# Kernel optimization log

Hardware: AMD Instinct MI355X
Metric: run time of the kernel (lower is better)

Reference implementation:

```python
import jax, jax.numpy as jnp
import numpy as np

N = 16384      # nodes per graph (128x128 image)
E = 9 * N      # 8-neighborhood + self edges
C = 512        # input feature channels
M = 32         # matrixSize


def _p(key, shape, scale=0.05):
    return jax.random.normal(key, shape, dtype=jnp.float32) * scale


def setup_inputs() -> dict:
    key = jax.random.key(0)
    ks = jax.random.split(key, 40)
    inp = {
        "cF": jax.random.normal(ks[0], (N, C), dtype=jnp.float32),
        "sF": jax.random.normal(ks[1], (N, C), dtype=jnp.float32),
        "content_edge_index": jax.random.randint(ks[2], (2, E), 0, N),
        "content_selections": jax.random.randint(ks[3], (E,), 0, 9),
        "style_edge_index": jax.random.randint(ks[4], (2, E), 0, N),
        "style_selections": jax.random.randint(ks[5], (E,), 0, 9),
        "compress_W": _p(ks[6], (1, C, M)),   # kernel_size=1 -> 1 selection
        "compress_b": _p(ks[7], (M,)),
        "unzip_W": _p(ks[8], (1, M, C)),
        "unzip_b": _p(ks[9], (C,)),
    }
    i = 10
    for net in ("cnet", "snet"):
        for j, (ci, co) in enumerate([(C, 256), (256, 128), (128, M)], 1):
            inp[f"{net}_W{j}"] = _p(ks[i], (9, ci, co)); i += 1  # kernel_size=3 -> 9 selections
            inp[f"{net}_b{j}"] = _p(ks[i], (co,)); i += 1
        inp[f"{net}_fcW"] = _p(ks[i], (M * M, M * M)); i += 1   # torch Linear [out,in]
        inp[f"{net}_fcb"] = _p(ks[i], (M * M,)); i += 1
    return inp


def sel_conv(x, edge_index, sel, W, b):
    """SelectionConv: per-selection weight, gather from src, scatter-add to dst.
    x: [N,Cin], W: [S,Cin,Cout]. Edges with selection >= S are masked (kernel_size=1)."""
    S = W.shape[0]
    t = jnp.einsum('nc,scd->snd', x, W)              # [S, N, Cout]
    src, dst = edge_index[0], edge_index[1]
    msgs = t[jnp.minimum(sel, S - 1), src]           # [E, Cout]
    msgs = jnp.where((sel < S)[:, None], msgs, 0.0)
    return jax.ops.segment_sum(msgs, dst, num_segments=x.shape[0]) + b


def cnn_net(x, ei, sel, W1, b1, W2, b2, W3, b3, fcW, fcb):
    h = jax.nn.relu(sel_conv(x, ei, sel, W1, b1))
    h = jax.nn.relu(sel_conv(h, ei, sel, W2, b2))
    h = sel_conv(h, ei, sel, W3, b3)                 # [N, M]
    g = (h.T @ h) / h.shape[0]                       # [M, M] gram
    return g.reshape(-1) @ fcW.T + fcb               # [M*M]


def reference(cF, sF, content_edge_index, content_selections, style_edge_index,
              style_selections, compress_W, compress_b, unzip_W, unzip_b,
              cnet_W1, cnet_b1, cnet_W2, cnet_b2, cnet_W3, cnet_b3, cnet_fcW, cnet_fcb,
              snet_W1, snet_b1, snet_W2, snet_b2, snet_W3, snet_b3, snet_fcW, snet_fcb):
    cMean = jnp.mean(cF, axis=0, keepdims=True)
    cFc = cF - cMean
    sMean = jnp.mean(sF, axis=0, keepdims=True)
    sFc = sF - sMean
    compress_content = sel_conv(cFc, content_edge_index, content_selections,
                                compress_W, compress_b)          # [N, M]
    m = compress_W.shape[2]
    cMat = cnn_net(cFc, content_edge_index, content_selections,
                   cnet_W1, cnet_b1, cnet_W2, cnet_b2, cnet_W3, cnet_b3,
                   cnet_fcW, cnet_fcb).reshape(m, m)
    sMat = cnn_net(sFc, style_edge_index, style_selections,
                   snet_W1, snet_b1, snet_W2, snet_b2, snet_W3, snet_b3,
                   snet_fcW, snet_fcb).reshape(m, m)
    transmatrix = sMat @ cMat                                    # [M, M]
    transfeature = (transmatrix @ compress_content.T).T          # [N, M]
    out = sel_conv(transfeature, content_edge_index, content_selections,
                   unzip_W, unzip_b) + sMean                     # [N, 512]
    return (out, transmatrix)
```

## Files before the change

### kernel.cpp

```cpp
#include <hip/hip_runtime.h>
#include <hip/hip_bf16.h>
#include <cstddef>
#include <cstdint>

#define NN 16384
#define EE (9*NN)
#define CC 512

typedef __attribute__((ext_vector_type(4))) float f32x4;
typedef __attribute__((ext_vector_type(8))) short bf16x8;

static inline int idiv(int a, int b){ return (a+b-1)/b; }

__device__ __forceinline__ float bf2f(unsigned short u){
    union{unsigned u; float f;} v; v.u = ((unsigned)u) << 16; return v.f;
}
__device__ __forceinline__ unsigned short f2bf(float f){
    union{float f; unsigned u;} v; v.f = f;
    unsigned r = v.u + 0x7fffu + ((v.u >> 16) & 1u);
    return (unsigned short)(r >> 16);
}

__device__ __forceinline__ void gload16(const void* gsrc, void* ldst){
    __builtin_amdgcn_global_load_lds(
        (const __attribute__((address_space(1))) unsigned int*)gsrc,
        (__attribute__((address_space(3))) unsigned int*)ldst,
        16, 0, 0);
}


__global__ void zero_i(int* __restrict__ p, int n){
    int i = blockIdx.x*256 + threadIdx.x; if (i < n) p[i] = 0;
}

__global__ void colsum2(const float* __restrict__ F0, float* __restrict__ cs0,
                        const float* __restrict__ F1, float* __restrict__ cs1){
    const float* F = blockIdx.z ? F1 : F0;
    float* cs = blockIdx.z ? cs1 : cs0;
    const int RPB = NN/256;
    int r0 = blockIdx.x * RPB;
    int c4 = threadIdx.x;
    float4 s = {0.f,0.f,0.f,0.f};
    for (int r = 0; r < RPB; ++r){
        float4 v = ((const float4*)(F + (size_t)(r0+r)*CC))[c4];
        s.x += v.x; s.y += v.y; s.z += v.z; s.w += v.w;
    }
    atomicAdd(&cs[c4*4+0], s.x);
    atomicAdd(&cs[c4*4+1], s.y);
    atomicAdd(&cs[c4*4+2], s.z);
    atomicAdd(&cs[c4*4+3], s.w);
}

__global__ void center2(const float* __restrict__ F0, const float* __restrict__ cs0,
                        ushort4* __restrict__ o0,
                        const float* __restrict__ F1, const float* __restrict__ cs1,
                        ushort4* __restrict__ o1){
    const float* F = blockIdx.z ? F1 : F0;
    const float* cs = blockIdx.z ? cs1 : cs0;
    ushort4* o = blockIdx.z ? o1 : o0;
    int i = blockIdx.x*256 + threadIdx.x;
    float4 v = ((const float4*)F)[i];
    int c = (i << 2) & (CC-1);
    float4 m = *(const float4*)(cs + c);
    ushort4 r;
    r.x = f2bf(v.x - m.x*(1.f/NN));
    r.y = f2bf(v.y - m.y*(1.f/NN));
    r.z = f2bf(v.z - m.z*(1.f/NN));
    r.w = f2bf(v.w - m.w*(1.f/NN));
    o[i] = r;
}

__global__ void wtransz(const float* __restrict__ W0, unsigned short* __restrict__ Wt0,
                        const float* __restrict__ W1, unsigned short* __restrict__ Wt1,
                        int S, int K, int Cout, int Npad, int Kpad){
    const float* W = blockIdx.z ? W1 : W0;
    unsigned short* Wt = blockIdx.z ? Wt1 : Wt0;
    int idx = blockIdx.x*256 + threadIdx.x;
    if (idx >= Npad*Kpad) return;
    int colp = idx / Kpad, k = idx - colp*Kpad;
    int s = colp / Cout, j = colp - s*Cout;
    float v = 0.f;
    if (s < S && k < K) v = W[((size_t)s*K + k)*Cout + j];
    Wt[idx] = f2bf(v);
}

__global__ void wtrans2z(const float* __restrict__ W0, const float* __restrict__ W1,
                         unsigned short* __restrict__ Wt0, unsigned short* __restrict__ Wt1,
                         int K, int Cout){
    __shared__ float tile[32][129];
    int s = blockIdx.z % 9;
    const float* W = (blockIdx.z < 9) ? W0 : W1;
    unsigned short* Wt = (blockIdx.z < 9) ? Wt0 : Wt1;
    int jb = blockIdx.x*128, kb = blockIdx.y*32;
    const float* Ws = W + (size_t)s*K*Cout;
    for (int r = 0; r < 32; ++r)
        tile[r][threadIdx.x] = Ws[(size_t)(kb+r)*Cout + jb + threadIdx.x];
    __syncthreads();
    int kk = threadIdx.x & 31, j0 = threadIdx.x >> 5;
    for (int jj = j0; jj < 128; jj += 4)
        Wt[(size_t)(s*Cout + jb + jj)*K + kb + kk] = f2bf(tile[kk][jj]);
}

__global__ void csr_count3(const int* __restrict__ cDst, const int* __restrict__ sDst,
                           const int* __restrict__ cSel,
                           int* __restrict__ cCnt, int* __restrict__ sCnt, int* __restrict__ cCnt0){
    int e = blockIdx.x*256 + threadIdx.x;
    if (e >= EE) return;
    int z = blockIdx.z;
    if (z == 0)      atomicAdd(&cCnt[cDst[e]], 1);
    else if (z == 1) atomicAdd(&sCnt[sDst[e]], 1);
    else if (cSel[e] == 0) atomicAdd(&cCnt0[cDst[e]], 1);
}
__global__ void csr_scan3(const int* __restrict__ c0, const int* __restrict__ c1,
                          const int* __restrict__ c2,
                          int* __restrict__ r0, int* __restrict__ r1, int* __restrict__ r2){
    const int* cnt = blockIdx.z==0 ? c0 : (blockIdx.z==1 ? c1 : c2);
    int* rowptr    = blockIdx.z==0 ? r0 : (blockIdx.z==1 ? r1 : r2);
    __shared__ int part[1024];
    int t = threadIdx.x;
    int base = t*16, s = 0;
    int local[16];
    #pragma unroll
    for (int i = 0; i < 16; ++i){ local[i] = s; s += cnt[base+i]; }
    part[t] = s; __syncthreads();
    for (int off = 1; off < 1024; off <<= 1){
        int v = (t >= off) ? part[t-off] : 0;
        __syncthreads();
        part[t] += v;
        __syncthreads();
    }
    int pre = (t == 0) ? 0 : part[t-1];
    #pragma unroll
    for (int i = 0; i < 16; ++i) rowptr[base+i] = pre + local[i];
    if (t == 1023) rowptr[NN] = part[1023];
}
__global__ void csr_fill3(const int* __restrict__ cSrc, const int* __restrict__ cDst,
                          const int* __restrict__ cSel,
                          const int* __restrict__ sSrc, const int* __restrict__ sDst,
                          const int* __restrict__ sSel,
                          const int* __restrict__ cRow, const int* __restrict__ sRow,
                          const int* __restrict__ cRow0,
                          int* __restrict__ cCur, int* __restrict__ sCur, int* __restrict__ cCur0,
                          int* __restrict__ cEl, int* __restrict__ sEl, int* __restrict__ cEl0){
    int e = blockIdx.x*256 + threadIdx.x;
    if (e >= EE) return;
    int z = blockIdx.z;
    if (z == 0){
        int d = cDst[e];
        int p = atomicAdd(&cCur[d], 1);
        cEl[cRow[d] + p] = (cSrc[e] << 4) | cSel[e];
    } else if (z == 1){
        int d = sDst[e];
        int p = atomicAdd(&sCur[d], 1);
        sEl[sRow[d] + p] = (sSrc[e] << 4) | sSel[e];
    } else if (cSel[e] == 0){
        int d = cDst[e];
        int p = atomicAdd(&cCur0[d], 1);
        cEl0[cRow0[d] + p] = cSrc[e];
    }
}

template<typename OutT>
__global__ __launch_bounds__(256, 2)
void mfma_gemm(const unsigned short* __restrict__ A0, const unsigned short* __restrict__ Bt0,
               OutT* __restrict__ C0,
               const unsigned short* __restrict__ A1, const unsigned short* __restrict__ Bt1,
               OutT* __restrict__ C1, int K, int N){
    const unsigned short* A  = blockIdx.z ? A1 : A0;
    const unsigned short* Bt = blockIdx.z ? Bt1 : Bt0;
    OutT* C = blockIdx.z ? C1 : C0;
    __shared__ __align__(16) unsigned short As[128*64];
    __shared__ __align__(16) unsigned short Bs[128*64];
    const int tid  = threadIdx.x;
    const int wave = tid >> 6, lane = tid & 63;
    const int row0 = blockIdx.y << 7, col0 = blockIdx.x << 7;
    const int wm = wave >> 1, wn = wave & 1;
    const int fr = lane & 15, fq = lane >> 4;
    f32x4 acc[4][4] = {};
    for (int k0 = 0; k0 < K; k0 += 64){
        __syncthreads();
        #pragma unroll
        for (int i = 0; i < 4; ++i){
            int chb = (wave*4 + i) * 64;
            int ch  = chb + lane;
            int r   = ch >> 3, c8 = ch & 7;
            gload16((const char*)(A  + (size_t)(row0 + r)*K + k0) + c8*16, As + chb*8);
            gload16((const char*)(Bt + (size_t)(col0 + r)*K + k0) + c8*16, Bs + chb*8);
        }
        __syncthreads();
        #pragma unroll
        for (int ks = 0; ks < 2; ++ks){
            bf16x8 av[4], bv[4];
            #pragma unroll
            for (int m = 0; m < 4; ++m)
                av[m] = *(const bf16x8*)(As + ((wm<<6)+(m<<4)+fr)*64 + (ks<<5) + (fq<<3));
            #pragma unroll
            for (int n = 0; n < 4; ++n)
                bv[n] = *(const bf16x8*)(Bs + ((wn<<6)+(n<<4)+fr)*64 + (ks<<5) + (fq<<3));
            #pragma unroll
            for (int m = 0; m < 4; ++m)
                #pragma unroll
                for (int n = 0; n < 4; ++n)
                    acc[m][n] = __builtin_amdgcn_mfma_f32_16x16x32_bf16(bv[n], av[m], acc[m][n], 0, 0, 0);
        }
    }
    #pragma unroll
    for (int m = 0; m < 4; ++m){
        int row = row0 + (wm<<6) + (m<<4) + fr;
        OutT* crow = C + (size_t)row*N + col0 + (wn<<6) + (fq<<2);
        #pragma unroll
        for (int n = 0; n < 4; ++n){
            if constexpr (sizeof(OutT) == 2){
                unsigned lo = f2bf(acc[m][n][0]) | ((unsigned)f2bf(acc[m][n][1]) << 16);
                unsigned hi = f2bf(acc[m][n][2]) | ((unsigned)f2bf(acc[m][n][3]) << 16);
                uint2 pk; pk.x = lo; pk.y = hi;
                *(uint2*)((unsigned short*)crow + (n<<4)) = pk;
            } else {
                float4 pk; pk.x = acc[m][n][0]; pk.y = acc[m][n][1];
                pk.z = acc[m][n][2]; pk.w = acc[m][n][3];
                *(float4*)((float*)crow + (n<<4)) = pk;
            }
        }
    }
}

template<int NT, typename OutT>
__global__ __launch_bounds__(256, 4)
void gemm_db(const unsigned short* __restrict__ A0, const unsigned short* __restrict__ Bt0,
             OutT* __restrict__ C0,
             const unsigned short* __restrict__ A1, const unsigned short* __restrict__ Bt1,
             OutT* __restrict__ C1, int N){
    constexpr int LDK = NT*32;
    const unsigned short* A  = blockIdx.z ? A1 : A0;
    const unsigned short* Bt = blockIdx.z ? Bt1 : Bt0;
    OutT* C = blockIdx.z ? C1 : C0;
    __shared__ __align__(16) unsigned short lds[2][2][4096];
    const int tid = threadIdx.x, w = tid >> 6, l = tid & 63;
    const int wm = w >> 1, wn = w & 1;
    const int fr = l & 15, fq = l >> 4;
    const int nbx = gridDim.x;
    const int nwg = gridDim.x * gridDim.y;
    int blin = blockIdx.y * nbx + blockIdx.x;
    int sw = (blin & 7) * (nwg >> 3) + (blin >> 3);
    const int bx = sw % nbx, by = sw / nbx;
    const int row0 = by << 7, col0 = bx << 7;

    const unsigned short* gA = A + (size_t)row0 * LDK;
    const unsigned short* gB = Bt + (size_t)col0 * LDK;

    auto STG = [&](int buf, int t){
        #pragma unroll
        for (int mtx = 0; mtx < 2; ++mtx){
            const unsigned short* gb = mtx ? gB : gA;
            #pragma unroll
            for (int ld = 0; ld < 2; ++ld){
                int o = (ld*256 + tid) * 16;
                int row = o >> 6;
                int kb = (o & 63) ^ (((o >> 7) & 3) << 4);
                gload16((const char*)(gb + (size_t)row*LDK + t*32) + kb,
                        (char*)&lds[buf][mtx][0] + o);
            }
        }
    };

    f32x4 acc[4][4] = {};
    STG(0, 0);
    __syncthreads();
    for (int t = 0; t < NT; ++t){
        int cur = t & 1;
        if (t + 1 < NT) STG(cur ^ 1, t + 1);
        bf16x8 av[4], bv[4];
        #pragma unroll
        for (int m = 0; m < 4; ++m){
            int r = wm*64 + m*16 + fr;
            int p = (r*64 + fq*16) ^ (((r >> 1) & 3) << 4);
            av[m] = *(const bf16x8*)((const char*)&lds[cur][0][0] + p);
        }
        #pragma unroll
        for (int n = 0; n < 4; ++n){
            int r = wn*64 + n*16 + fr;
            int p = (r*64 + fq*16) ^ (((r >> 1) & 3) << 4);
            bv[n] = *(const bf16x8*)((const char*)&lds[cur][1][0] + p);
        }
        #pragma unroll
        for (int m = 0; m < 4; ++m)
            #pragma unroll
            for (int n = 0; n < 4; ++n)
                acc[m][n] = __builtin_amdgcn_mfma_f32_16x16x32_bf16(bv[n], av[m], acc[m][n], 0, 0, 0);
        __syncthreads();
    }

    #pragma unroll
    for (int m = 0; m < 4; ++m){
        int row = row0 + wm*64 + m*16 + fr;
        OutT* crow = C + (size_t)row*N + col0 + (wn<<6) + (fq<<2);
        #pragma unroll
        for (int n = 0; n < 4; ++n){
            if constexpr (sizeof(OutT) == 2){
                unsigned lo = f2bf(acc[m][n][0]) | ((unsigned)f2bf(acc[m][n][1]) << 16);
                unsigned hi = f2bf(acc[m][n][2]) | ((unsigned)f2bf(acc[m][n][3]) << 16);
                uint2 pk; pk.x = lo; pk.y = hi;
                *(uint2*)((unsigned short*)crow + (n<<4)) = pk;
            } else {
                float4 pk; pk.x = acc[m][n][0]; pk.y = acc[m][n][1];
                pk.z = acc[m][n][2]; pk.w = acc[m][n][3];
                *(float4*)((float*)crow + (n<<4)) = pk;
            }
        }
    }
}

template<typename TO, bool RELU>
__global__ void gather8z(const int* __restrict__ rp0, const int* __restrict__ el0,
                         const unsigned short* __restrict__ t0, const float* __restrict__ b0,
                         TO* __restrict__ o0,
                         const int* __restrict__ rp1, const int* __restrict__ el1,
                         const unsigned short* __restrict__ t1, const float* __restrict__ b1,
                         TO* __restrict__ o1,
                         int tStride, int coutShift){
    const int* rowptr = blockIdx.z ? rp1 : rp0;
    const int* elist  = blockIdx.z ? el1 : el0;
    const unsigned short* t = blockIdx.z ? t1 : t0;
    const float* bias = blockIdx.z ? b1 : b0;
    TO* out = blockIdx.z ? o1 : o0;
    int idx = blockIdx.x*256 + threadIdx.x;
    int chSh = coutShift - 3;
    int d = idx >> chSh;
    int c0 = (idx & ((1 << chSh) - 1)) << 3;
    float acc[8];
    {
        const float4* bb = (const float4*)(bias + c0);
        float4 a = bb[0], b = bb[1];
        acc[0]=a.x; acc[1]=a.y; acc[2]=a.z; acc[3]=a.w;
        acc[4]=b.x; acc[5]=b.y; acc[6]=b.z; acc[7]=b.w;
    }
    int j1 = rowptr[d+1];
    #pragma unroll 2
    for (int j = rowptr[d]; j < j1; ++j){
        int p = elist[j];
        int s = p & 15, sr = p >> 4;
        bf16x8 v = *(const bf16x8*)(t + (size_t)sr*tStride + (s << coutShift) + c0);
        #pragma unroll
        for (int k = 0; k < 8; ++k) acc[k] += bf2f((unsigned short)v[k]);
    }
    if (RELU){
        #pragma unroll
        for (int k = 0; k < 8; ++k) acc[k] = fmaxf(acc[k], 0.f);
    }
    if constexpr (sizeof(TO) == 2){
        union { bf16x8 v; unsigned short u[8]; } r;
        #pragma unroll
        for (int k = 0; k < 8; ++k) r.u[k] = f2bf(acc[k]);
        *(bf16x8*)((unsigned short*)out + ((size_t)d << coutShift) + c0) = r.v;
    } else {
        float4 a = {acc[0],acc[1],acc[2],acc[3]};
        float4 b = {acc[4],acc[5],acc[6],acc[7]};
        float4* op = (float4*)((float*)out + ((size_t)d << coutShift) + c0);
        op[0] = a; op[1] = b;
    }
}

template<bool ADDV>
__global__ void gather4f(const int* __restrict__ rowptr, const int* __restrict__ elist,
                         const float* __restrict__ t,
                         const float* __restrict__ bias, const float* __restrict__ addvec,
                         float* __restrict__ out, int tStride, int coutShift){
    int idx = blockIdx.x*256 + threadIdx.x;
    int chSh = coutShift - 2;
    int d = idx >> chSh;
    int c0 = (idx & ((1 << chSh) - 1)) << 2;
    float4 bb = *(const float4*)(bias + c0);
    float acc0 = bb.x, acc1 = bb.y, acc2 = bb.z, acc3 = bb.w;
    if (ADDV){
        float4 av = *(const float4*)(addvec + c0);
        acc0 += av.x*(1.f/NN); acc1 += av.y*(1.f/NN);
        acc2 += av.z*(1.f/NN); acc3 += av.w*(1.f/NN);
    }
    int j1 = rowptr[d+1];
    #pragma unroll 2
    for (int j = rowptr[d]; j < j1; ++j){
        int sr = elist[j];
        float4 v = *(const float4*)(t + (size_t)sr*tStride + c0);
        acc0 += v.x; acc1 += v.y; acc2 += v.z; acc3 += v.w;
    }
    float4 r = {acc0, acc1, acc2, acc3};
    *(float4*)(out + ((size_t)d << coutShift) + c0) = r;
}

__global__ void gram2(const float* __restrict__ h0, float* __restrict__ g0,
                      const float* __restrict__ h1, float* __restrict__ g1){
    const float* h = blockIdx.z ? h1 : h0;
    float* g = blockIdx.z ? g1 : g0;
    const int RPB = NN/64;
    int r0 = blockIdx.x*RPB;
    int i = threadIdx.x >> 5, j = threadIdx.x & 31;
    float s = 0.f;
    for (int r = 0; r < RPB; ++r){
        const float* row = h + (size_t)(r0+r)*32;
        s += row[i]*row[j];
    }
    atomicAdd(&g[threadIdx.x], s);
}

__global__ void fc2(const float* __restrict__ g0, const float* __restrict__ fcW0,
                    const float* __restrict__ fcb0, float* __restrict__ o0,
                    const float* __restrict__ g1, const float* __restrict__ fcW1,
                    const float* __restrict__ fcb1, float* __restrict__ o1){
    const float* g   = blockIdx.z ? g1 : g0;
    const float* fcW = blockIdx.z ? fcW1 : fcW0;
    const float* fcb = blockIdx.z ? fcb1 : fcb0;
    float* outMat    = blockIdx.z ? o1 : o0;
    int i = blockIdx.x;
    float s = 0.f;
    for (int j = threadIdx.x; j < 1024; j += 256)
        s += g[j] * (1.f/NN) * fcW[(size_t)i*1024 + j];
    __shared__ float red[256];
    red[threadIdx.x] = s; __syncthreads();
    for (int off = 128; off > 0; off >>= 1){
        if (threadIdx.x < off) red[threadIdx.x] += red[threadIdx.x+off];
        __syncthreads();
    }
    if (threadIdx.x == 0) outMat[i] = red[0] + fcb[i];
}

__global__ void mm32_kernel(const float* __restrict__ A, const float* __restrict__ B,
                            float* __restrict__ T){
    int i = threadIdx.x >> 5, j = threadIdx.x & 31;
    float s = 0.f;
    for (int k = 0; k < 32; ++k) s += A[i*32+k]*B[k*32+j];
    T[threadIdx.x] = s;
}

__global__ void tf_cvt_kernel(const float* __restrict__ cc, const float* __restrict__ T,
                              unsigned short* __restrict__ tfbB){
    __shared__ float Ts[1024];
    for (int i = threadIdx.x; i < 1024; i += blockDim.x) Ts[i] = T[i];
    __syncthreads();
    int idx = blockIdx.x*blockDim.x + threadIdx.x;
    int n = idx >> 5, i = idx & 31;
    float s = 0.f;
    const float* crow = cc + (size_t)n*32;
    #pragma unroll
    for (int j = 0; j < 32; ++j) s += crow[j] * Ts[i*32+j];
    tfbB[(size_t)n*64 + i] = f2bf(s);
    tfbB[(size_t)n*64 + 32 + i] = 0;
}

extern "C" void kernel_launch(void* const* d_in, const int* in_sizes, int n_in,
                              void* d_out, int out_size, void* d_ws, size_t ws_size,
                              hipStream_t stream){
    const float* cF   = (const float*)d_in[0];
    const float* sF   = (const float*)d_in[1];
    const int*   cEI  = (const int*)d_in[2];
    const int*   cSel = (const int*)d_in[3];
    const int*   sEI  = (const int*)d_in[4];
    const int*   sSel = (const int*)d_in[5];
    const float* compW= (const float*)d_in[6];
    const float* compB= (const float*)d_in[7];
    const float* unzW = (const float*)d_in[8];
    const float* unzB = (const float*)d_in[9];
    const float* cW1=(const float*)d_in[10]; const float* cB1=(const float*)d_in[11];
    const float* cW2=(const float*)d_in[12]; const float* cB2=(const float*)d_in[13];
    const float* cW3=(const float*)d_in[14]; const float* cB3=(const float*)d_in[15];
    const float* cFW=(const float*)d_in[16]; const float* cFB=(const float*)d_in[17];
    const float* sW1=(const float*)d_in[18]; const float* sB1=(const float*)d_in[19];
    const float* sW2=(const float*)d_in[20]; const float* sB2=(const float*)d_in[21];
    const float* sW3=(const float*)d_in[22]; const float* sB3=(const float*)d_in[23];
    const float* sFW=(const float*)d_in[24]; const float* sFB=(const float*)d_in[25];

    float* out  = (float*)d_out;
    float* Tmat = out + (size_t)NN*CC;

    char* w = (char*)d_ws;
    auto alloc = [&](size_t b)->char*{ char* p = w; w += (b + 255) & ~(size_t)255; return p; };
    float* cCol = (float*)alloc(512*4);
    float* sCol = (float*)alloc(512*4);
    float* cg   = (float*)alloc(1024*4);
    float* sg   = (float*)alloc(1024*4);
    float* cMat = (float*)alloc(1024*4);
    float* sMat = (float*)alloc(1024*4);
    int* cCnt = (int*)alloc(NN*4);
    int* cCur = (int*)alloc(NN*4);
    int* sCnt = (int*)alloc(NN*4);
    int* sCur = (int*)alloc(NN*4);
    int* cCnt0= (int*)alloc(NN*4);
    int* cCur0= (int*)alloc(NN*4);
    int* cRow = (int*)alloc((NN+1)*4);
    int* sRow = (int*)alloc((NN+1)*4);
    int* cRow0= (int*)alloc((NN+1)*4);
    int* cEl  = (int*)alloc(EE*4);
    int* sEl  = (int*)alloc(EE*4);
    int* cEl0 = (int*)alloc(EE*4);
    float* ccbuf = (float*)alloc((size_t)NN*32*4);
    unsigned short* tfbB = (unsigned short*)alloc((size_t)NN*64*2);
    unsigned short* wtC1 = (unsigned short*)alloc((size_t)2304*512*2);
    unsigned short* wtC2 = (unsigned short*)alloc((size_t)1280*256*2);
    unsigned short* wtC3 = (unsigned short*)alloc((size_t)384*128*2);
    unsigned short* wtS1 = (unsigned short*)alloc((size_t)2304*512*2);
    unsigned short* wtS2 = (unsigned short*)alloc((size_t)1280*256*2);
    unsigned short* wtS3 = (unsigned short*)alloc((size_t)384*128*2);
    unsigned short* wtCo = (unsigned short*)alloc((size_t)128*512*2);
    unsigned short* wtU  = (unsigned short*)alloc((size_t)512*64*2);
    unsigned short* cFcB = (unsigned short*)alloc((size_t)NN*512*2);
    unsigned short* sFcB = (unsigned short*)alloc((size_t)NN*512*2);
    float* h3c = (float*)alloc((size_t)NN*32*4);
    float* h3s = (float*)alloc((size_t)NN*32*4);
    unsigned short* tC = (unsigned short*)alloc((size_t)NN*2304*2);
    unsigned short* tS = (unsigned short*)alloc((size_t)NN*2304*2);
    float* tFc = (float*)tC;
    unsigned short* h1c = cFcB;
    unsigned short* h1s = sFcB;
    unsigned short* h2c = cFcB + (size_t)NN*256;
    unsigned short* h2s = sFcB + (size_t)NN*256;

    const int* cSrc = cEI; const int* cDst = cEI + EE;
    const int* sSrc = sEI; const int* sDst = sEI + EE;

    int zeroInts = (int)(((char*)cCur0 - (char*)d_ws)/4) + NN;
    zero_i<<<idiv(zeroInts,256),256,0,stream>>>((int*)d_ws, zeroInts);

    colsum2<<<dim3(256,1,2),128,0,stream>>>(cF, cCol, sF, sCol);
    center2<<<dim3(NN*CC/1024,1,2),256,0,stream>>>(cF, cCol, (ushort4*)cFcB,
                                                   sF, sCol, (ushort4*)sFcB);

    wtrans2z<<<dim3(2,16,18),128,0,stream>>>(cW1, sW1, wtC1, wtS1, 512, 256);
    wtrans2z<<<dim3(1,8,18),128,0,stream>>>(cW2, sW2, wtC2, wtS2, 256, 128);
    wtransz<<<dim3(idiv(384*128,256),1,2),256,0,stream>>>(cW3, wtC3, sW3, wtS3, 9,128,32, 384,128);
    wtransz<<<dim3(idiv(128*512,256),1,1),256,0,stream>>>(compW, wtCo, compW, wtCo, 1,512,32, 128,512);
    wtransz<<<dim3(idiv(512*64,256),1,1),256,0,stream>>>(unzW, wtU, unzW, wtU, 1,32,512, 512,64);

    csr_count3<<<dim3(idiv(EE,256),1,3),256,0,stream>>>(cDst, sDst, cSel, cCnt, sCnt, cCnt0);
    csr_scan3<<<dim3(1,1,3),1024,0,stream>>>(cCnt, sCnt, cCnt0, cRow, sRow, cRow0);
    csr_fill3<<<dim3(idiv(EE,256),1,3),256,0,stream>>>(cSrc,cDst,cSel, sSrc,sDst,sSel,
                                                       cRow,sRow,cRow0, cCur,sCur,cCur0,
                                                       cEl,sEl,cEl0);

    mfma_gemm<float><<<dim3(1,128,1),256,0,stream>>>(cFcB, wtCo, tFc,
                                                     cFcB, wtCo, tFc, 512, 128);
    gather4f<false><<<NN*8/256,256,0,stream>>>(cRow0,cEl0,tFc,compB,nullptr,ccbuf,128,5);

    gemm_db<16,unsigned short><<<dim3(18,128,2),256,0,stream>>>(cFcB, wtC1, tC,
                                                                sFcB, wtS1, tS, 2304);
    gather8z<unsigned short,true><<<dim3(2048,1,2),256,0,stream>>>(
        cRow,cEl,tC,cB1,h1c, sRow,sEl,tS,sB1,h1s, 2304, 8);
    gemm_db<8,unsigned short><<<dim3(10,128,2),256,0,stream>>>(h1c, wtC2, tC,
                                                               h1s, wtS2, tS, 1280);
    gather8z<unsigned short,true><<<dim3(1024,1,2),256,0,stream>>>(
        cRow,cEl,tC,cB2,h2c, sRow,sEl,tS,sB2,h2s, 1280, 7);
    mfma_gemm<unsigned short><<<dim3(3,128,2),256,0,stream>>>(h2c, wtC3, tC,
                                                              h2s, wtS3, tS, 128, 384);
    gather8z<float,false><<<dim3(256,1,2),256,0,stream>>>(
        cRow,cEl,tC,cB3,h3c, sRow,sEl,tS,sB3,h3s, 384, 5);
    gram2<<<dim3(64,1,2),1024,0,stream>>>(h3c, cg, h3s, sg);
    fc2<<<dim3(1024,1,2),256,0,stream>>>(cg,cFW,cFB,cMat, sg,sFW,sFB,sMat);

    mm32_kernel<<<1,1024,0,stream>>>(sMat, cMat, Tmat);
    tf_cvt_kernel<<<NN*32/256,256,0,stream>>>(ccbuf, Tmat, tfbB);

    mfma_gemm<float><<<dim3(4,128,1),256,0,stream>>>(tfbB, wtU, tFc,
                                                     tfbB, wtU, tFc, 64, 512);
    gather4f<true><<<NN*128/256,256,0,stream>>>(cRow0,cEl0,tFc,unzB,sCol,out,512,9);
}
```

Before: 407.9 us.

## Reorder unzip stage: aggregate compressed features first, fold transmatrix into unzip weights

Because the unzip convolution uses a single selection, the neighbourhood aggregation is linear and commutes with the per-node transform. The change therefore aggregates the 32-wide compressed-content features over edges first. It then folds the 32x32 transmatrix into the 32x512 unzip weight and computes the output with one dense fp32 kernel that also adds the bias and style mean. This replaces the bf16 GEMM plus a 512-wide edge gather, which read large intermediates, with a 32-wide gather and a compute-light dense pass. It also raises the occupancy hint on the double-buffered GEMM from 4 to 5 waves per SIMD, which may cost registers.

```diff
diff --git a/kernel.cpp b/kernel.cpp
--- a/kernel.cpp
+++ b/kernel.cpp
@@ -225,7 +225,7 @@
 }
 
 template<int NT, typename OutT>
-__global__ __launch_bounds__(256, 4)
+__global__ __launch_bounds__(256, 5)
 void gemm_db(const unsigned short* __restrict__ A0, const unsigned short* __restrict__ Bt0,
              OutT* __restrict__ C0,
              const unsigned short* __restrict__ A1, const unsigned short* __restrict__ Bt1,
@@ -423,27 +423,67 @@
     if (threadIdx.x == 0) outMat[i] = red[0] + fcb[i];
 }
 
-__global__ void mm32_kernel(const float* __restrict__ A, const float* __restrict__ B,
-                            float* __restrict__ T){
-    int i = threadIdx.x >> 5, j = threadIdx.x & 31;
-    float s = 0.f;
-    for (int k = 0; k < 32; ++k) s += A[i*32+k]*B[k*32+j];
-    T[threadIdx.x] = s;
-}
-
-__global__ void tf_cvt_kernel(const float* __restrict__ cc, const float* __restrict__ T,
-                              unsigned short* __restrict__ tfbB){
+__global__ void mm32tu(const float* __restrict__ sM, const float* __restrict__ cM,
+                       const float* __restrict__ Uw, float* __restrict__ Tout,
+                       float* __restrict__ TU){
     __shared__ float Ts[1024];
-    for (int i = threadIdx.x; i < 1024; i += blockDim.x) Ts[i] = T[i];
+    int t = threadIdx.x;
+    for (int e = t; e < 1024; e += 512){
+        int i = e >> 5, j = e & 31;
+        float s = 0.f;
+        #pragma unroll
+        for (int k = 0; k < 32; ++k) s += sM[i*32+k]*cM[k*32+j];
+        Ts[e] = s;
+        Tout[e] = s;
+    }
     __syncthreads();
-    int idx = blockIdx.x*blockDim.x + threadIdx.x;
-    int n = idx >> 5, i = idx & 31;
-    float s = 0.f;
-    const float* crow = cc + (size_t)n*32;
+    float u[32];
     #pragma unroll
-    for (int j = 0; j < 32; ++j) s += crow[j] * Ts[i*32+j];
-    tfbB[(size_t)n*64 + i] = f2bf(s);
-    tfbB[(size_t)n*64 + 32 + i] = 0;
+    for (int i = 0; i < 32; ++i) u[i] = Uw[i*512 + t];
+    for (int j = 0; j < 32; ++j){
+        float s = 0.f;
+        #pragma unroll
+        for (int i = 0; i < 32; ++i) s += Ts[i*32+j] * u[i];
+        TU[j*512 + t] = s;
+    }
+}
+
+__global__ __launch_bounds__(256, 4)
+void unzip_out(const float* __restrict__ agg, const float* __restrict__ TU,
+               const float* __restrict__ unzB, const float* __restrict__ scs,
+               float* __restrict__ out){
+    __shared__ float TUl[32][256];
+    __shared__ float aggL[16][32];
+    int tid = threadIdx.x;
+    int r0 = blockIdx.x * 16;
+    int col0 = blockIdx.y * 256;
+    for (int i = tid; i < 2048; i += 256){
+        int j = i >> 6, cg = i & 63;
+        ((float4*)&TUl[j][0])[cg] = *(const float4*)(TU + j*512 + col0 + (cg<<2));
+    }
+    if (tid < 128)
+        ((float4*)&aggL[0][0])[tid] =
+            *(const float4*)(agg + (size_t)(r0 + (tid>>3))*32 + ((tid&7)<<2));
+    __syncthreads();
+    #pragma unroll
+    for (int rp = 0; rp < 4; ++rp){
+        int r = rp*4 + (tid >> 6);
+        int c = (tid & 63) << 2;
+        float4 b = *(const float4*)(unzB + col0 + c);
+        float4 sm = *(const float4*)(scs + col0 + c);
+        float a0 = b.x + sm.x*(1.f/NN);
+        float a1 = b.y + sm.y*(1.f/NN);
+        float a2 = b.z + sm.z*(1.f/NN);
+        float a3 = b.w + sm.w*(1.f/NN);
+        #pragma unroll
+        for (int j = 0; j < 32; ++j){
+            float av = aggL[r][j];
+            const float* tur = &TUl[j][c];
+            a0 += av*tur[0]; a1 += av*tur[1]; a2 += av*tur[2]; a3 += av*tur[3];
+        }
+        float4 o = {a0,a1,a2,a3};
+        *(float4*)(out + (size_t)(r0 + r)*512 + col0 + c) = o;
+    }
 }
 
 extern "C" void kernel_launch(void* const* d_in, const int* in_sizes, int n_in,
@@ -479,6 +519,7 @@
     float* sg   = (float*)alloc(1024*4);
     float* cMat = (float*)alloc(1024*4);
     float* sMat = (float*)alloc(1024*4);
+    float* zpad = (float*)alloc(32*4);
     int* cCnt = (int*)alloc(NN*4);
     int* cCur = (int*)alloc(NN*4);
     int* sCnt = (int*)alloc(NN*4);
@@ -492,7 +533,8 @@
     int* sEl  = (int*)alloc(EE*4);
     int* cEl0 = (int*)alloc(EE*4);
     float* ccbuf = (float*)alloc((size_t)NN*32*4);
-    unsigned short* tfbB = (unsigned short*)alloc((size_t)NN*64*2);
+    float* aggb  = (float*)alloc((size_t)NN*32*4);
+    float* TU    = (float*)alloc((size_t)32*512*4);
     unsigned short* wtC1 = (unsigned short*)alloc((size_t)2304*512*2);
     unsigned short* wtC2 = (unsigned short*)alloc((size_t)1280*256*2);
     unsigned short* wtC3 = (unsigned short*)alloc((size_t)384*128*2);
@@ -500,7 +542,6 @@
     unsigned short* wtS2 = (unsigned short*)alloc((size_t)1280*256*2);
     unsigned short* wtS3 = (unsigned short*)alloc((size_t)384*128*2);
     unsigned short* wtCo = (unsigned short*)alloc((size_t)128*512*2);
-    unsigned short* wtU  = (unsigned short*)alloc((size_t)512*64*2);
     unsigned short* cFcB = (unsigned short*)alloc((size_t)NN*512*2);
     unsigned short* sFcB = (unsigned short*)alloc((size_t)NN*512*2);
     float* h3c = (float*)alloc((size_t)NN*32*4);
@@ -527,7 +568,6 @@
     wtrans2z<<<dim3(1,8,18),128,0,stream>>>(cW2, sW2, wtC2, wtS2, 256, 128);
     wtransz<<<dim3(idiv(384*128,256),1,2),256,0,stream>>>(cW3, wtC3, sW3, wtS3, 9,128,32, 384,128);
     wtransz<<<dim3(idiv(128*512,256),1,1),256,0,stream>>>(compW, wtCo, compW, wtCo, 1,512,32, 128,512);
-    wtransz<<<dim3(idiv(512*64,256),1,1),256,0,stream>>>(unzW, wtU, unzW, wtU, 1,32,512, 512,64);
 
     csr_count3<<<dim3(idiv(EE,256),1,3),256,0,stream>>>(cDst, sDst, cSel, cCnt, sCnt, cCnt0);
     csr_scan3<<<dim3(1,1,3),1024,0,stream>>>(cCnt, sCnt, cCnt0, cRow, sRow, cRow0);
@@ -538,6 +578,8 @@
     mfma_gemm<float><<<dim3(1,128,1),256,0,stream>>>(cFcB, wtCo, tFc,
                                                      cFcB, wtCo, tFc, 512, 128);
     gather4f<false><<<NN*8/256,256,0,stream>>>(cRow0,cEl0,tFc,compB,nullptr,ccbuf,128,5);
+
+    gather4f<false><<<NN*8/256,256,0,stream>>>(cRow0,cEl0,ccbuf,zpad,nullptr,aggb,32,5);
 
     gemm_db<16,unsigned short><<<dim3(18,128,2),256,0,stream>>>(cFcB, wtC1, tC,
                                                                 sFcB, wtS1, tS, 2304);
@@ -554,10 +596,6 @@
     gram2<<<dim3(64,1,2),1024,0,stream>>>(h3c, cg, h3s, sg);
     fc2<<<dim3(1024,1,2),256,0,stream>>>(cg,cFW,cFB,cMat, sg,sFW,sFB,sMat);
 
-    mm32_kernel<<<1,1024,0,stream>>>(sMat, cMat, Tmat);
-    tf_cvt_kernel<<<NN*32/256,256,0,stream>>>(ccbuf, Tmat, tfbB);
-
-    mfma_gemm<float><<<dim3(4,128,1),256,0,stream>>>(tfbB, wtU, tFc,
-                                                     tfbB, wtU, tFc, 64, 512);
-    gather4f<true><<<NN*128/256,256,0,stream>>>(cRow0,cEl0,tFc,unzB,sCol,out,512,9);
-}
+    mm32tu<<<1,512,0,stream>>>(sMat, cMat, unzW, Tmat, TU);
+    unzip_out<<<dim3(NN/16,2),256,0,stream>>>(aggb, TU, unzB, sCol, out);
+}
```

Result: slower. 1.121 ms (+174.8%).
